# Kernel tuning notes

Measured on AMD Instinct MI355X. Metric: run time of the kernel, lower is better.

## Reference

```python
import jax, jax.numpy as jnp
import numpy as np
import math

MAX_LEN = 65536
NUM_HEADS = 16
HEAD_DIM = 64
K_MAX = 64
LOCAL_WINDOW = 512
LOG_N = math.ceil(math.log2(MAX_LEN + 1))   # 17
LEAF_START = 2 ** LOG_N                      # segment-tree leaf offset


def cover_set(pos):
    """O(log n) segment-tree nodes covering prefix [0..pos-1], each with leaf-depth."""
    if pos <= 0:
        return []
    l, r = LEAF_START, LEAF_START + min(pos, MAX_LEN)
    out = []
    while l < r:
        if l & 1:
            out.append((l, LOG_N - int(math.floor(math.log2(l)))))
            l += 1
        if r & 1:
            r -= 1
            out.append((r, LOG_N - int(math.floor(math.log2(r)))))
        l >>= 1
        r >>= 1
    return out


def node_content(v_tokens, node_idx, depth):
    """Content of a FULL subtree node under the concat/pairwise-mean gated merge.
    Equals: concat tokens while K<=k_max, then (left+right)/2 elementwise, which
    collapses to a strided mean over chunks of size L//K_MAX. Returns (H, K, D)."""
    L = 1 << depth
    a = (node_idx << depth) - LEAF_START          # first token covered by node
    chunk = v_tokens[a:a + L]                     # (L, H, D), static slice
    if L <= K_MAX:
        f = chunk                                 # (L, H, D)
    else:
        f = chunk.reshape(L // K_MAX, K_MAX, NUM_HEADS, HEAD_DIM).mean(0)  # (K_MAX,H,D)
    return jnp.transpose(f, (1, 0, 2))            # (H, K, D)


def setup_inputs() -> dict:
    key = jax.random.key(0)
    k1, k2, k3 = jax.random.split(key, 3)
    v_tokens = jax.random.normal(k1, (50000, NUM_HEADS, HEAD_DIM), jnp.float32)
    q_new = jax.random.normal(k2, (1, NUM_HEADS, HEAD_DIM), jnp.float32)
    depth_proj_w = jax.random.normal(k3, (LOG_N + 1, HEAD_DIM, HEAD_DIM), jnp.float32) * 0.02
    depth_temp = jnp.linspace(0.5, 4.0, LOG_N + 1).astype(jnp.float32)
    return {"v_tokens": v_tokens, "q_new": q_new, "depth_proj_w": depth_proj_w,
            "depth_temp": depth_temp, "n_tokens": 50000}


def reference(v_tokens, q_new, depth_proj_w, depth_temp, n_tokens):
    pos = int(n_tokens)
    q = q_new[0]                                   # (H, D)
    inv_sqrt_d = 1.0 / math.sqrt(HEAD_DIM)

    # --- local window attention over last min(pos, W) tokens (chronological) ---
    n_local = min(pos, LOCAL_WINDOW)
    v_local = v_tokens[pos - n_local:pos]          # (W, H, D)
    s = jnp.einsum('hd,khd->hk', q, v_local) * inv_sqrt_d
    w = jax.nn.softmax(s, axis=-1)
    local_out = jnp.einsum('hk,khd->hd', w, v_local)   # (H, D)

    # --- multi-depth causal tree attention over the O(log n) cover set ---
    node_outs = []
    for node_idx, depth in cover_set(pos):
        f = node_content(v_tokens, node_idx, depth)    # (H, K, D)
        q_depth = q + q @ depth_proj_w[depth].T        # depth-specific query delta
        scale = 1.0 / ((jax.nn.softplus(depth_temp[depth]) + 1e-6) * math.sqrt(HEAD_DIM))
        s = jnp.einsum('hd,hkd->hk', q_depth, f) * scale
        w = jnp.einsum('hk,hkd->hd', jax.nn.softmax(s, axis=-1), f)
        node_outs.append(w)
    if node_outs:
        tree_out = jnp.stack(node_outs, axis=0).mean(0)
    else:
        tree_out = jnp.zeros_like(local_out)

    return (local_out + tree_out)[None]            # (1, H, D)
```

## Files before the change

### kernel.cpp

```cpp
#include <hip/hip_runtime.h>
#include <math.h>

#define NUM_HEADS   16
#define HEAD_DIM    64
#define KMAXN       64
#define LOCAL_WIN   512
#define LOG_N       17
#define LEAF_START  131072
#define MAX_LEN_TOK 65536
#define ROW         1024
#define SLICE       65536
#define MAXN        34

typedef float vf4 __attribute__((ext_vector_type(4)));

__device__ __forceinline__ vf4 ntload(const float* p) {
    return __builtin_nontemporal_load((const vf4*)p);
}

__device__ __forceinline__ void attn_tile(const float* __restrict__ bp, int CB, float invC,
                                          int K, int dep, int h,
                                          const float* __restrict__ q,
                                          const float* __restrict__ W,
                                          const float* __restrict__ temp,
                                          float* __restrict__ node_out_row,
                                          float (&fh)[64][64], float* qs, float* qds,
                                          float* sv, float* ps, float (&red)[4][64]) {
    int tid = threadIdx.x, lane = tid & 63, w = tid >> 6;
    if (tid < 64) qs[tid] = q[h * 64 + tid];
    for (int id = tid; id < 1024; id += 256) {
        int r = id >> 4, c4 = (id & 15) << 2;
        if (r < K) {
            vf4 s0 = 0.f, s1 = 0.f, s2 = 0.f, s3 = 0.f;
            const float* p = bp + (long)r * ROW + c4;
            int cb = 0;
            for (; cb + 4 <= CB; cb += 4) {
                s0 += *(const vf4*)(p + (long)cb * SLICE);
                s1 += *(const vf4*)(p + (long)(cb + 1) * SLICE);
                s2 += *(const vf4*)(p + (long)(cb + 2) * SLICE);
                s3 += *(const vf4*)(p + (long)(cb + 3) * SLICE);
            }
            for (; cb < CB; ++cb) s0 += *(const vf4*)(p + (long)cb * SLICE);
            s0 += s1; s2 += s3; s0 += s2;
            s0 *= invC;
            *(vf4*)&fh[r][c4] = s0;
        }
    }
    __syncthreads();

    float qp = 0.f;
    const float* Wr = W + ((long)dep * 64 + lane) * 64;
    #pragma unroll
    for (int e = w * 16; e < w * 16 + 16; ++e) qp += qs[e] * Wr[e];
    red[w][lane] = qp;
    __syncthreads();
    if (w == 0) qds[lane] = qs[lane] + red[0][lane] + red[1][lane] + red[2][lane] + red[3][lane];
    __syncthreads();
    float qd    = qds[lane];
    float sp    = log1pf(expf(temp[dep]));
    float scale = 1.0f / ((sp + 1e-6f) * 8.0f);

    for (int k = w; k < K; k += 4) {
        float p2 = qd * fh[k][lane];
        #pragma unroll
        for (int m = 1; m < 64; m <<= 1) p2 += __shfl_xor(p2, m, 64);
        if (lane == 0) sv[k] = p2 * scale;
    }
    __syncthreads();

    if (w == 0) {
        float s  = (lane < K) ? sv[lane] : -1e30f;
        float mx = s;
        #pragma unroll
        for (int m = 1; m < 64; m <<= 1) mx = fmaxf(mx, __shfl_xor(mx, m, 64));
        float e = (lane < K) ? expf(s - mx) : 0.f;
        float S = e;
        #pragma unroll
        for (int m = 1; m < 64; m <<= 1) S += __shfl_xor(S, m, 64);
        ps[lane] = e / S;
    }
    __syncthreads();

    float o = 0.f;
    for (int k = w; k < K; k += 4) o += ps[k] * fh[k][lane];
    red[w][lane] = o;
    __syncthreads();
    if (w == 0)
        node_out_row[lane] = red[0][lane] + red[1][lane] + red[2][lane] + red[3][lane];
}

struct KAArgs {
    int nPart, bbK1, nDirect, pos;
    int offLocal, offCnt, offNodeOut;
    int a1[MAXN], cpb1[MAXN], C1[MAXN], off1[MAXN], bbase[MAXN];
    int aD[MAXN], CD[MAXN], KD[MAXN], depD[MAXN], idxD[MAXN];
};

__global__ __launch_bounds__(256, 4) void kA(const float* __restrict__ v,
                                             const float* __restrict__ q,
                                             const float* __restrict__ W,
                                             const float* __restrict__ temp,
                                             float* __restrict__ ws, KAArgs A) {
    __shared__ float fh[64][64];
    __shared__ float qs[64], qds[64], sv[64], ps[64];
    __shared__ float red[4][64];
    __shared__ float sc[LOCAL_WIN];
    __shared__ float wred[8];
    __shared__ float mS[2];

    int b = blockIdx.x, tid = threadIdx.x;
    int lane = tid & 63, w = tid >> 6;
    if (b == 0 && tid == 0) *((unsigned*)(ws + A.offCnt)) = 0u;

    if (b < A.bbK1) {
        int node = 0;
        for (int i = 1; i < A.nPart; ++i) if (b >= A.bbase[i]) node = i;
        int lb = b - A.bbase[node];
        int cb = lb >> 4, kg = lb & 15, k0 = kg << 2;
        int c0 = cb * A.cpb1[node];
        int c1 = c0 + A.cpb1[node];
        if (c1 > A.C1[node]) c1 = A.C1[node];
        int j4 = tid * 4;

        vf4 acc0 = 0.f, acc1 = 0.f, acc2 = 0.f, acc3 = 0.f;
        int c = c0;
        for (; c + 2 <= c1; c += 2) {
            const float* p0 = v + (long)(A.a1[node] + c * 64 + k0) * ROW + j4;
            const float* p1 = p0 + SLICE;
            vf4 y0 = ntload(p0);
            vf4 y1 = ntload(p0 + ROW);
            vf4 y2 = ntload(p0 + 2 * ROW);
            vf4 y3 = ntload(p0 + 3 * ROW);
            vf4 z0 = ntload(p1);
            vf4 z1 = ntload(p1 + ROW);
            vf4 z2 = ntload(p1 + 2 * ROW);
            vf4 z3 = ntload(p1 + 3 * ROW);
            acc0 += y0 + z0; acc1 += y1 + z1; acc2 += y2 + z2; acc3 += y3 + z3;
        }
        if (c < c1) {
            const float* p0 = v + (long)(A.a1[node] + c * 64 + k0) * ROW + j4;
            acc0 += ntload(p0);
            acc1 += ntload(p0 + ROW);
            acc2 += ntload(p0 + 2 * ROW);
            acc3 += ntload(p0 + 3 * ROW);
        }
        float* wp = ws + (long)A.off1[node] + (long)cb * SLICE + (long)k0 * ROW + j4;
        *(vf4*)(wp)           = acc0;
        *(vf4*)(wp + ROW)     = acc1;
        *(vf4*)(wp + 2 * ROW) = acc2;
        *(vf4*)(wp + 3 * ROW) = acc3;
    } else if (b < A.bbK1 + NUM_HEADS) {
        int h    = b - A.bbK1;
        int nloc = A.pos < LOCAL_WIN ? A.pos : LOCAL_WIN;
        int t0   = A.pos - nloc;

        if (tid < 64) qs[tid] = q[h * 64 + tid];
        __syncthreads();

        float s0 = -1e30f, s1 = -1e30f;
        if (tid < nloc) {
            const float* vr = v + (long)(t0 + tid) * ROW + h * 64;
            float acc = 0.f;
            #pragma unroll 8
            for (int d = 0; d < 64; ++d) acc += qs[d] * vr[d];
            s0 = acc * 0.125f;
        }
        if (tid + 256 < nloc) {
            const float* vr = v + (long)(t0 + tid + 256) * ROW + h * 64;
            float acc = 0.f;
            #pragma unroll 8
            for (int d = 0; d < 64; ++d) acc += qs[d] * vr[d];
            s1 = acc * 0.125f;
        }
        float mx = fmaxf(s0, s1);
        #pragma unroll
        for (int m = 1; m < 64; m <<= 1) mx = fmaxf(mx, __shfl_xor(mx, m, 64));
        if (lane == 0) wred[w] = mx;
        __syncthreads();
        if (tid == 0) {
            float m2 = wred[0];
            for (int i = 1; i < 4; ++i) m2 = fmaxf(m2, wred[i]);
            mS[0] = m2;
        }
        __syncthreads();
        float m = mS[0];

        float e0 = (tid < nloc)       ? expf(s0 - m) : 0.f;
        float e1 = (tid + 256 < nloc) ? expf(s1 - m) : 0.f;
        sc[tid]       = e0;
        sc[tid + 256] = e1;
        float su = e0 + e1;
        #pragma unroll
        for (int mm = 1; mm < 64; mm <<= 1) su += __shfl_xor(su, mm, 64);
        if (lane == 0) wred[4 + w] = su;
        __syncthreads();
        if (tid == 0) {
            float S2 = 0.f;
            for (int i = 0; i < 4; ++i) S2 += wred[4 + i];
            mS[1] = S2;
        }
        __syncthreads();
        float S = mS[1];

        float acc = 0.f;
        {
            const float* vb = v + (long)t0 * ROW + h * 64 + lane;
            int tb = w * 128;
            #pragma unroll 4
            for (int i = 0; i < 128; ++i) {
                int t = tb + i;
                if (t < nloc) acc += sc[t] * vb[(long)t * ROW];
            }
        }
        red[w][lane] = acc;
        __syncthreads();
        if (w == 0) {
            float tot = red[0][lane] + red[1][lane] + red[2][lane] + red[3][lane];
            (ws + A.offLocal)[h * 64 + lane] = (nloc > 0) ? tot / S : 0.f;
        }
    } else {
        int t = b - A.bbK1 - NUM_HEADS;
        int d = t >> 4, h = t & 15;
        attn_tile(v + (long)A.aD[d] * ROW + h * 64, A.CD[d], 1.0f / (float)A.CD[d],
                  A.KD[d], A.depD[d], h, q, W, temp,
                  ws + A.offNodeOut + (long)A.idxD[d] * ROW + h * 64,
                  fh, qs, qds, sv, ps, red);
    }
}

struct KBArgs {
    int nPart, nNodes, nTiles;
    int offLocal, offCnt, offNodeOut;
    int C1[MAXN], CB1[MAXN], off1[MAXN], dep1[MAXN], idx1[MAXN];
};

__global__ __launch_bounds__(256, 4) void kB(const float* __restrict__ q,
                                             const float* __restrict__ W,
                                             const float* __restrict__ temp,
                                             float* __restrict__ ws,
                                             float* __restrict__ out, KBArgs B) {
    __shared__ float fh[64][64];
    __shared__ float qs[64], qds[64], sv[64], ps[64];
    __shared__ float red[4][64];
    __shared__ unsigned lastflag;

    int t = blockIdx.x, tid = threadIdx.x;
    int p = t >> 4, h = t & 15;
    float* node_out = ws + B.offNodeOut;

    attn_tile(ws + (long)B.off1[p] + h * 64, B.CB1[p], 1.0f / (float)B.C1[p],
              64, B.dep1[p], h, q, W, temp,
              node_out + (long)B.idx1[p] * ROW + h * 64,
              fh, qs, qds, sv, ps, red);

    __syncthreads();
    if (tid == 0) {
        __threadfence();
        unsigned old = atomicAdd((unsigned*)(ws + B.offCnt), 1u);
        lastflag = (old == (unsigned)(B.nTiles - 1)) ? 1u : 0u;
    }
    __syncthreads();
    if (lastflag) {
        __threadfence();
        const float* local_out = ws + B.offLocal;
        float invN = 1.0f / (float)B.nNodes;
        for (int i = tid; i < ROW; i += 256) {
            float tr = 0.f;
            for (int n = 0; n < B.nNodes; ++n) tr += node_out[(long)n * ROW + i];
            out[i] = local_out[i] + tr * invN;
        }
    }
}

__global__ __launch_bounds__(256) void k3_combine(const float* __restrict__ node_out,
                                                  const float* __restrict__ local_out,
                                                  int nNodes,
                                                  float* __restrict__ out) {
    int i = blockIdx.x * 256 + threadIdx.x;
    float tr = 0.f;
    for (int n = 0; n < nNodes; ++n) tr += node_out[(long)n * ROW + i];
    if (nNodes > 0) tr /= (float)nNodes;
    out[i] = local_out[i] + tr;
}

static int floor_log2_host(unsigned x) { int r = 0; while (x >>= 1) ++r; return r; }

extern "C" void kernel_launch(void* const* d_in, const int* in_sizes, int n_in,
                              void* d_out, int out_size, void* d_ws, size_t ws_size,
                              hipStream_t stream) {
    const float* v    = (const float*)d_in[0];
    const float* q    = (const float*)d_in[1];
    const float* W    = (const float*)d_in[2];
    const float* temp = (const float*)d_in[3];
    float* out        = (float*)d_out;
    float* ws         = (float*)d_ws;

    int pos = in_sizes[0] / ROW;

    int n_nodes = 0;
    int nv[MAXN], nd[MAXN];
    if (pos > 0) {
        long l = LEAF_START;
        long r = LEAF_START + (pos < MAX_LEN_TOK ? pos : MAX_LEN_TOK);
        while (l < r) {
            if (l & 1) { nv[n_nodes] = (int)l; nd[n_nodes] = LOG_N - floor_log2_host((unsigned)l); ++n_nodes; ++l; }
            if (r & 1) { --r; nv[n_nodes] = (int)r; nd[n_nodes] = LOG_N - floor_log2_host((unsigned)r); ++n_nodes; }
            l >>= 1; r >>= 1;
        }
    }

    int cpb_choice = 1024;
    for (int cand : {32, 64, 128, 256, 512, 1024}) {
        long tot_cb = 0;
        for (int i = 0; i < n_nodes; ++i) {
            int L = 1 << nd[i];
            int C = (L > KMAXN) ? L / KMAXN : 1;
            if (C > 8) tot_cb += (C + cand - 1) / cand;
        }
        long need = (tot_cb * (long)SLICE + (long)n_nodes * ROW + ROW + 64) * 4;
        if (need <= (long)ws_size) { cpb_choice = cand; break; }
    }

    KAArgs A{}; KBArgs B{};
    A.pos = pos;
    B.nNodes = n_nodes;
    int off = 0, bb = 0, nPart = 0, nDirect = 0;
    for (int i = 0; i < n_nodes; ++i) {
        int depth = nd[i];
        int L = 1 << depth;
        int a = (nv[i] << depth) - LEAF_START;
        int K = (L < KMAXN) ? L : KMAXN;
        int C = (L > KMAXN) ? L / KMAXN : 1;
        if (C > 8) {
            int CB  = (C + cpb_choice - 1) / cpb_choice;
            int cpb = (C + CB - 1) / CB;
            A.a1[nPart] = a; A.cpb1[nPart] = cpb; A.C1[nPart] = C;
            A.off1[nPart] = off; A.bbase[nPart] = bb;
            B.C1[nPart] = C; B.CB1[nPart] = CB; B.off1[nPart] = off;
            B.dep1[nPart] = depth; B.idx1[nPart] = i;
            off += CB * SLICE;
            bb  += 16 * CB;
            ++nPart;
        } else {
            A.aD[nDirect] = a; A.CD[nDirect] = C; A.KD[nDirect] = K;
            A.depD[nDirect] = depth; A.idxD[nDirect] = i;
            ++nDirect;
        }
    }
    A.nPart = nPart; A.bbK1 = bb; A.nDirect = nDirect;
    B.nPart = nPart; B.nTiles = nPart * NUM_HEADS;
    A.offNodeOut = off;
    A.offLocal   = off + n_nodes * ROW;
    A.offCnt     = A.offLocal + ROW;
    B.offNodeOut = A.offNodeOut; B.offLocal = A.offLocal; B.offCnt = A.offCnt;

    int gridA = bb + NUM_HEADS + nDirect * NUM_HEADS;
    hipLaunchKernelGGL(kA, dim3(gridA), dim3(256), 0, stream, v, q, W, temp, ws, A);

    if (nPart > 0) {
        hipLaunchKernelGGL(kB, dim3(B.nTiles), dim3(256), 0, stream,
                           q, W, temp, ws, out, B);
    } else {
        hipLaunchKernelGGL(k3_combine, dim3(4), dim3(256), 0, stream,
                           ws + (long)A.offNodeOut, ws + (long)A.offLocal, n_nodes, out);
    }
}
```

Before: 302.0 us.

## Rebalance partial-sum blocks, widen finalize kernel, and split combine into separate launch

The partial-sum blocks in kA now each cover 2 rows instead of 4, with twice as many blocks and a 4-chunk unrolled load loop. Nodes with C between 2 and 8 now go through the partial-sum path instead of the direct path. kB becomes a 512-thread kernel on a 2D grid that only computes node outputs, and the atomic last-block combine is replaced by a separate k3_combine launch. The goal is more memory parallelism in the reduction and no atomic/fence serialization, at the cost of an extra kernel launch and more blocks.

```diff
diff --git a/kernel.cpp b/kernel.cpp
--- a/kernel.cpp
+++ b/kernel.cpp
@@ -18,14 +18,14 @@
     return __builtin_nontemporal_load((const vf4*)p);
 }
 
-__device__ __forceinline__ void attn_tile(const float* __restrict__ bp, int CB, float invC,
-                                          int K, int dep, int h,
-                                          const float* __restrict__ q,
-                                          const float* __restrict__ W,
-                                          const float* __restrict__ temp,
-                                          float* __restrict__ node_out_row,
-                                          float (&fh)[64][64], float* qs, float* qds,
-                                          float* sv, float* ps, float (&red)[4][64]) {
+__device__ __forceinline__ void attn_tile256(const float* __restrict__ bp, int CB, float invC,
+                                             int K, int dep, int h,
+                                             const float* __restrict__ q,
+                                             const float* __restrict__ W,
+                                             const float* __restrict__ temp,
+                                             float* __restrict__ node_out_row,
+                                             float (&fh)[64][64], float* qs, float* qds,
+                                             float* sv, float* ps, float (&red)[4][64]) {
     int tid = threadIdx.x, lane = tid & 63, w = tid >> 6;
     if (tid < 64) qs[tid] = q[h * 64 + tid];
     for (int id = tid; id < 1024; id += 256) {
@@ -91,9 +91,9 @@
 
 struct KAArgs {
     int nPart, bbK1, nDirect, pos;
-    int offLocal, offCnt, offNodeOut;
+    int offLocal, offNodeOut;
     int a1[MAXN], cpb1[MAXN], C1[MAXN], off1[MAXN], bbase[MAXN];
-    int aD[MAXN], CD[MAXN], KD[MAXN], depD[MAXN], idxD[MAXN];
+    int aD[MAXN], KD[MAXN], depD[MAXN], idxD[MAXN];
 };
 
 __global__ __launch_bounds__(256, 4) void kA(const float* __restrict__ v,
@@ -110,45 +110,43 @@
 
     int b = blockIdx.x, tid = threadIdx.x;
     int lane = tid & 63, w = tid >> 6;
-    if (b == 0 && tid == 0) *((unsigned*)(ws + A.offCnt)) = 0u;
 
     if (b < A.bbK1) {
         int node = 0;
         for (int i = 1; i < A.nPart; ++i) if (b >= A.bbase[i]) node = i;
         int lb = b - A.bbase[node];
-        int cb = lb >> 4, kg = lb & 15, k0 = kg << 2;
+        int cb = lb >> 5;
+        int kg = lb & 31;
+        int k0 = kg * 2;
         int c0 = cb * A.cpb1[node];
         int c1 = c0 + A.cpb1[node];
         if (c1 > A.C1[node]) c1 = A.C1[node];
+        int a  = A.a1[node];
         int j4 = tid * 4;
 
-        vf4 acc0 = 0.f, acc1 = 0.f, acc2 = 0.f, acc3 = 0.f;
+        vf4 acc0 = 0.f, acc1 = 0.f;
         int c = c0;
-        for (; c + 2 <= c1; c += 2) {
-            const float* p0 = v + (long)(A.a1[node] + c * 64 + k0) * ROW + j4;
-            const float* p1 = p0 + SLICE;
+        for (; c + 4 <= c1; c += 4) {
+            const float* p0 = v + (long)(a + c * 64 + k0) * ROW + j4;
             vf4 y0 = ntload(p0);
             vf4 y1 = ntload(p0 + ROW);
-            vf4 y2 = ntload(p0 + 2 * ROW);
-            vf4 y3 = ntload(p0 + 3 * ROW);
-            vf4 z0 = ntload(p1);
-            vf4 z1 = ntload(p1 + ROW);
-            vf4 z2 = ntload(p1 + 2 * ROW);
-            vf4 z3 = ntload(p1 + 3 * ROW);
-            acc0 += y0 + z0; acc1 += y1 + z1; acc2 += y2 + z2; acc3 += y3 + z3;
-        }
-        if (c < c1) {
-            const float* p0 = v + (long)(A.a1[node] + c * 64 + k0) * ROW + j4;
+            vf4 y2 = ntload(p0 + SLICE);
+            vf4 y3 = ntload(p0 + SLICE + ROW);
+            vf4 y4 = ntload(p0 + 2 * SLICE);
+            vf4 y5 = ntload(p0 + 2 * SLICE + ROW);
+            vf4 y6 = ntload(p0 + 3 * SLICE);
+            vf4 y7 = ntload(p0 + 3 * SLICE + ROW);
+            acc0 += y0 + y2 + y4 + y6;
+            acc1 += y1 + y3 + y5 + y7;
+        }
+        for (; c < c1; ++c) {
+            const float* p0 = v + (long)(a + c * 64 + k0) * ROW + j4;
             acc0 += ntload(p0);
             acc1 += ntload(p0 + ROW);
-            acc2 += ntload(p0 + 2 * ROW);
-            acc3 += ntload(p0 + 3 * ROW);
         }
         float* wp = ws + (long)A.off1[node] + (long)cb * SLICE + (long)k0 * ROW + j4;
-        *(vf4*)(wp)           = acc0;
-        *(vf4*)(wp + ROW)     = acc1;
-        *(vf4*)(wp + 2 * ROW) = acc2;
-        *(vf4*)(wp + 3 * ROW) = acc3;
+        *(vf4*)(wp)       = acc0;
+        *(vf4*)(wp + ROW) = acc1;
     } else if (b < A.bbK1 + NUM_HEADS) {
         int h    = b - A.bbK1;
         int nloc = A.pos < LOCAL_WIN ? A.pos : LOCAL_WIN;
@@ -221,54 +219,106 @@
     } else {
         int t = b - A.bbK1 - NUM_HEADS;
         int d = t >> 4, h = t & 15;
-        attn_tile(v + (long)A.aD[d] * ROW + h * 64, A.CD[d], 1.0f / (float)A.CD[d],
-                  A.KD[d], A.depD[d], h, q, W, temp,
-                  ws + A.offNodeOut + (long)A.idxD[d] * ROW + h * 64,
-                  fh, qs, qds, sv, ps, red);
+        attn_tile256(v + (long)A.aD[d] * ROW + h * 64, 1, 1.0f,
+                     A.KD[d], A.depD[d], h, q, W, temp,
+                     ws + A.offNodeOut + (long)A.idxD[d] * ROW + h * 64,
+                     fh, qs, qds, sv, ps, red);
     }
 }
 
 struct KBArgs {
-    int nPart, nNodes, nTiles;
-    int offLocal, offCnt, offNodeOut;
+    int nBig;
     int C1[MAXN], CB1[MAXN], off1[MAXN], dep1[MAXN], idx1[MAXN];
 };
 
-__global__ __launch_bounds__(256, 4) void kB(const float* __restrict__ q,
-                                             const float* __restrict__ W,
-                                             const float* __restrict__ temp,
-                                             float* __restrict__ ws,
-                                             float* __restrict__ out, KBArgs B) {
+__global__ __launch_bounds__(512) void kB(const float* __restrict__ ws,
+                                          const float* __restrict__ q,
+                                          const float* __restrict__ W,
+                                          const float* __restrict__ temp,
+                                          float* __restrict__ node_out, KBArgs B) {
+    int h   = blockIdx.x;
+    int p   = blockIdx.y;
+    int tid = threadIdx.x;
+    int lane = tid & 63;
+    int w    = tid >> 6;
+
     __shared__ float fh[64][64];
     __shared__ float qs[64], qds[64], sv[64], ps[64];
-    __shared__ float red[4][64];
-    __shared__ unsigned lastflag;
-
-    int t = blockIdx.x, tid = threadIdx.x;
-    int p = t >> 4, h = t & 15;
-    float* node_out = ws + B.offNodeOut;
-
-    attn_tile(ws + (long)B.off1[p] + h * 64, B.CB1[p], 1.0f / (float)B.C1[p],
-              64, B.dep1[p], h, q, W, temp,
-              node_out + (long)B.idx1[p] * ROW + h * 64,
-              fh, qs, qds, sv, ps, red);
-
-    __syncthreads();
-    if (tid == 0) {
-        __threadfence();
-        unsigned old = atomicAdd((unsigned*)(ws + B.offCnt), 1u);
-        lastflag = (old == (unsigned)(B.nTiles - 1)) ? 1u : 0u;
-    }
-    __syncthreads();
-    if (lastflag) {
-        __threadfence();
-        const float* local_out = ws + B.offLocal;
-        float invN = 1.0f / (float)B.nNodes;
-        for (int i = tid; i < ROW; i += 256) {
-            float tr = 0.f;
-            for (int n = 0; n < B.nNodes; ++n) tr += node_out[(long)n * ROW + i];
-            out[i] = local_out[i] + tr * invN;
-        }
+    __shared__ float red[8][64];
+
+    if (tid < 64) qs[tid] = q[h * 64 + tid];
+
+    const float* bp = ws + (long)B.off1[p] + h * 64;
+    int   CB   = B.CB1[p];
+    float invC = 1.0f / (float)B.C1[p];
+
+    for (int id = tid; id < 1024; id += 512) {
+        int r  = id >> 4;
+        int c4 = (id & 15) << 2;
+        vf4 s0 = 0.f, s1 = 0.f, s2 = 0.f, s3 = 0.f;
+        const float* pp = bp + (long)r * ROW + c4;
+        int cb = 0;
+        for (; cb + 4 <= CB; cb += 4) {
+            s0 += *(const vf4*)(pp + (long)cb * SLICE);
+            s1 += *(const vf4*)(pp + (long)(cb + 1) * SLICE);
+            s2 += *(const vf4*)(pp + (long)(cb + 2) * SLICE);
+            s3 += *(const vf4*)(pp + (long)(cb + 3) * SLICE);
+        }
+        for (; cb < CB; ++cb) s0 += *(const vf4*)(pp + (long)cb * SLICE);
+        s0 += s1; s2 += s3; s0 += s2;
+        s0 *= invC;
+        *(vf4*)&fh[r][c4] = s0;
+    }
+    __syncthreads();
+
+    int dep = B.dep1[p];
+    float qp = 0.f;
+    const float* Wr = W + ((long)dep * 64 + lane) * 64;
+    #pragma unroll
+    for (int e = w * 8; e < w * 8 + 8; ++e) qp += qs[e] * Wr[e];
+    red[w][lane] = qp;
+    __syncthreads();
+    if (w == 0) {
+        float t = qs[lane];
+        #pragma unroll
+        for (int i = 0; i < 8; ++i) t += red[i][lane];
+        qds[lane] = t;
+    }
+    __syncthreads();
+    float qd    = qds[lane];
+    float sp    = log1pf(expf(temp[dep]));
+    float scale = 1.0f / ((sp + 1e-6f) * 8.0f);
+
+    for (int k = w; k < 64; k += 8) {
+        float p2 = qd * fh[k][lane];
+        #pragma unroll
+        for (int m = 1; m < 64; m <<= 1) p2 += __shfl_xor(p2, m, 64);
+        if (lane == 0) sv[k] = p2 * scale;
+    }
+    __syncthreads();
+
+    if (w == 0) {
+        float s  = sv[lane];
+        float mx = s;
+        #pragma unroll
+        for (int m = 1; m < 64; m <<= 1) mx = fmaxf(mx, __shfl_xor(mx, m, 64));
+        float e = expf(s - mx);
+        float S = e;
+        #pragma unroll
+        for (int m = 1; m < 64; m <<= 1) S += __shfl_xor(S, m, 64);
+        ps[lane] = e / S;
+    }
+    __syncthreads();
+
+    float o = 0.f;
+    for (int k = w; k < 64; k += 8) o += ps[k] * fh[k][lane];
+    red[w][lane] = o;
+    __syncthreads();
+    if (w == 0) {
+        float t = 0.f;
+        #pragma unroll
+        for (int i = 0; i < 8; ++i) t += red[i][lane];
+        node_out[(long)B.idx1[p] * ROW + h * 64 + lane] = t;
     }
 }
 
@@ -315,53 +365,52 @@
         for (int i = 0; i < n_nodes; ++i) {
             int L = 1 << nd[i];
             int C = (L > KMAXN) ? L / KMAXN : 1;
-            if (C > 8) tot_cb += (C + cand - 1) / cand;
-        }
-        long need = (tot_cb * (long)SLICE + (long)n_nodes * ROW + ROW + 64) * 4;
+            if (C > 1) tot_cb += (C + cand - 1) / cand;
+        }
+        long need = (tot_cb * (long)SLICE + (long)n_nodes * ROW + ROW) * 4;
         if (need <= (long)ws_size) { cpb_choice = cand; break; }
     }
 
     KAArgs A{}; KBArgs B{};
     A.pos = pos;
-    B.nNodes = n_nodes;
-    int off = 0, bb = 0, nPart = 0, nDirect = 0;
+    int off = 0, bb = 0, nBig = 0, nDirect = 0;
     for (int i = 0; i < n_nodes; ++i) {
         int depth = nd[i];
         int L = 1 << depth;
         int a = (nv[i] << depth) - LEAF_START;
         int K = (L < KMAXN) ? L : KMAXN;
         int C = (L > KMAXN) ? L / KMAXN : 1;
-        if (C > 8) {
+        if (C > 1) {
             int CB  = (C + cpb_choice - 1) / cpb_choice;
             int cpb = (C + CB - 1) / CB;
-            A.a1[nPart] = a; A.cpb1[nPart] = cpb; A.C1[nPart] = C;
-            A.off1[nPart] = off; A.bbase[nPart] = bb;
-            B.C1[nPart] = C; B.CB1[nPart] = CB; B.off1[nPart] = off;
-            B.dep1[nPart] = depth; B.idx1[nPart] = i;
+            A.a1[nBig] = a; A.cpb1[nBig] = cpb; A.C1[nBig] = C;
+            A.off1[nBig] = off; A.bbase[nBig] = bb;
+            B.C1[nBig] = C; B.CB1[nBig] = CB; B.off1[nBig] = off;
+            B.dep1[nBig] = depth; B.idx1[nBig] = i;
             off += CB * SLICE;
-            bb  += 16 * CB;
-            ++nPart;
+            bb  += 32 * CB;
+            ++nBig;
         } else {
-            A.aD[nDirect] = a; A.CD[nDirect] = C; A.KD[nDirect] = K;
+            A.aD[nDirect] = a; A.KD[nDirect] = K;
             A.depD[nDirect] = depth; A.idxD[nDirect] = i;
             ++nDirect;
         }
     }
-    A.nPart = nPart; A.bbK1 = bb; A.nDirect = nDirect;
-    B.nPart = nPart; B.nTiles = nPart * NUM_HEADS;
+    A.nPart = nBig; A.bbK1 = bb; A.nDirect = nDirect;
+    B.nBig = nBig;
     A.offNodeOut = off;
     A.offLocal   = off + n_nodes * ROW;
-    A.offCnt     = A.offLocal + ROW;
-    B.offNodeOut = A.offNodeOut; B.offLocal = A.offLocal; B.offCnt = A.offCnt;
+
+    float* node_outp  = ws + (long)A.offNodeOut;
+    float* local_outp = ws + (long)A.offLocal;
 
     int gridA = bb + NUM_HEADS + nDirect * NUM_HEADS;
     hipLaunchKernelGGL(kA, dim3(gridA), dim3(256), 0, stream, v, q, W, temp, ws, A);
 
-    if (nPart > 0) {
-        hipLaunchKernelGGL(kB, dim3(B.nTiles), dim3(256), 0, stream,
-                           q, W, temp, ws, out, B);
-    } else {
-        hipLaunchKernelGGL(k3_combine, dim3(4), dim3(256), 0, stream,
-                           ws + (long)A.offNodeOut, ws + (long)A.offLocal, n_nodes, out);
-    }
-}
+    if (nBig > 0)
+        hipLaunchKernelGGL(kB, dim3(NUM_HEADS, nBig), dim3(512), 0, stream,
+                           ws, q, W, temp, node_outp, B);
+
+    hipLaunchKernelGGL(k3_combine, dim3(4), dim3(256), 0, stream,
+                       node_outp, local_outp, n_nodes, out);
+}
```

Measured after the change: 305.0 us. Within noise of the previous version (+1.0%).
